# Kernel optimization log

Measured on AMD Instinct MI355X. Metric: run time of the kernel, lower is better.

## Reference

```python
import jax, jax.numpy as jnp
import numpy as np

# GLIF3 / AlphaPSC constants from the module __init__
V_TH = -45.0      # v_threshold
V_RESET = -60.0   # v_reset (also used as leak reversal E_L)
C_M = 2.0         # membrane capacitance
TAU = 20.0        # membrane time constant
TAU_REF = 2.0     # refractory period (ms)
K = np.array([0.1, 0.2], dtype=np.float32)          # after-spike-current decay rates
ASC_AMPS = np.array([1.0, -2.0], dtype=np.float32)  # after-spike-current jump amplitudes
TAU_SYN = 5.0     # alpha synapse time constant
DT = 1.0

T, B, NI, NH, NO = 1000, 32, 512, 1024, 256


def setup_inputs() -> dict:
    key = jax.random.key(0)
    k1, k2, k3, k4 = jax.random.split(key, 4)
    x = jax.random.normal(k1, (T, B, NI), dtype=jnp.float32)
    # fc_in scaled up so injected current actually drives spiking from v_reset to v_threshold
    W_in = jax.random.normal(k2, (NH, NI), dtype=jnp.float32) * (50.0 / np.sqrt(NI))
    W_rec = jax.random.normal(k3, (NH, NH), dtype=jnp.float32) * (1.0 / np.sqrt(NH))
    W_out = jax.random.normal(k4, (NO, NH), dtype=jnp.float32) * (1.0 / np.sqrt(NH))
    return {"x": x, "W_in": W_in, "W_rec": W_rec, "W_out": W_out}


def _spike_fn(v):
    # Heaviside forward, sigmoid surrogate gradient (straight-through)
    soft = jax.nn.sigmoid(4.0 * (v - V_TH))
    hard = (v >= V_TH).astype(v.dtype)
    return soft + jax.lax.stop_gradient(hard - soft)


def reference(x, W_in, W_rec, W_out):
    # fc_in: [T,B,NI] @ [NH,NI]^T -> external current per step [T,B,NH]
    I_ext = jnp.einsum('tbi,hi->tbh', x, W_in)

    decay_syn = jnp.float32(np.exp(-DT / TAU_SYN))
    asc_decay = jnp.exp(-jnp.asarray(K) * DT)          # (2,)
    asc_amps = jnp.asarray(ASC_AMPS)                   # (2,)

    v0 = jnp.full((B, NH), V_RESET, dtype=jnp.float32)
    asc0 = jnp.zeros((2, B, NH), dtype=jnp.float32)
    ref0 = jnp.zeros((B, NH), dtype=jnp.float32)
    h0 = jnp.zeros((B, NH), dtype=jnp.float32)
    psc0 = jnp.zeros((B, NH), dtype=jnp.float32)

    def step(carry, I_t):
        v, asc, ref, h, psc = carry
        I = I_t + psc                                   # external + recurrent synaptic current
        asc = asc * asc_decay[:, None, None]            # after-spike currents decay
        # GLIF membrane update: C dv/dt = -C/tau (v - E_L) + I + sum(asc)
        v = v + DT * ((V_RESET - v) / TAU + (I + asc.sum(0)) / C_M)
        in_ref = ref > 0.0
        v = jnp.where(in_ref, V_RESET, v)               # clamp during refractory
        spike = _spike_fn(v) * (1.0 - in_ref.astype(v.dtype))
        v = v * (1.0 - spike) + V_RESET * spike         # hard reset on spike
        asc = asc + spike[None] * asc_amps[:, None, None]
        ref = jnp.where(spike > 0.5, TAU_REF, jnp.maximum(ref - DT, 0.0))
        # DenseConn recurrent projection of spikes, then AlphaPSC two-state filter
        rec = spike @ W_rec.T
        h = decay_syn * h + rec
        psc = decay_syn * psc + DT * h
        return (v, asc, ref, h, psc), spike

    _, spikes = jax.lax.scan(step, (v0, asc0, ref0, h0, psc0), I_ext)  # spikes: [T,B,NH]
    rate = spikes.mean(axis=0)                          # [B,NH]
    return rate @ W_out.T                               # [B,NO]
```

## Files before the change

kernel.cpp:

```cpp
#include <hip/hip_runtime.h>
#include <stdint.h>

#define T_STEPS 1000
#define B_SZ    32
#define NI      512
#define NH      1024
#define NO      256

#define NSLICE  8
#define NBLK    (B_SZ * NSLICE)

#define NHP     (NH + 16)
#define DUMMY   NH
#define BOFF    544

typedef unsigned long long u64;

#define OFF_IEXT 0ull
#define SZ_IEXT  ((unsigned long long)T_STEPS * B_SZ * NH * 4ull)
#define OFF_WTS  (OFF_IEXT + SZ_IEXT)
#define SZ_WTS   ((unsigned long long)NSLICE * NHP * 128 * 4ull)
#define OFF_RATE (OFF_WTS + SZ_WTS)
#define SZ_RATE  ((unsigned long long)B_SZ * NH * 4ull)
#define OFF_SYNC (OFF_RATE + SZ_RATE)
#define SZ_SYNC  ((unsigned long long)2 * B_SZ * NSLICE * 4 * 8ull)

__device__ __forceinline__ u64 ld64_agent(const u64* p) {
  return __hip_atomic_load(p, __ATOMIC_RELAXED, __HIP_MEMORY_SCOPE_AGENT);
}
__device__ __forceinline__ void st64_agent(u64* p, u64 v) {
  __hip_atomic_store(p, v, __ATOMIC_RELAXED, __HIP_MEMORY_SCOPE_AGENT);
}

__global__ __launch_bounds__(256) void prep_wts(const float* __restrict__ Wrec,
                                                float* __restrict__ WTS) {
  __shared__ float tile[64][65];
  const int tid = threadIdx.x;
  const int j0 = blockIdx.x * 64;
  const int i0 = blockIdx.y * 64;
  const int sl = j0 >> 7;
  const int jjb = j0 & 127;
#pragma unroll
  for (int k = 0; k < 16; ++k) {
    const int idx = k * 256 + tid;
    const int jl = idx >> 6, il = idx & 63;
    tile[jl][il] = Wrec[(size_t)(j0 + jl) * NH + i0 + il];
  }
  __syncthreads();
#pragma unroll
  for (int k = 0; k < 16; ++k) {
    const int idx = k * 256 + tid;
    const int il = idx >> 6, jl = idx & 63;
    WTS[((size_t)(sl * NHP + i0 + il)) * 128 + jjb + jl] = tile[jl][il];
  }
}

#define GBM 128
#define GBN 128
#define GBK 16
__global__ __launch_bounds__(256) void gemm_in(const float* __restrict__ X,
                                               const float* __restrict__ Win,
                                               float* __restrict__ I) {
  __shared__ float As[GBK][GBM + 4];
  __shared__ float Bs[GBK][GBN + 4];
  const int tid = threadIdx.x;
  const int m0 = blockIdx.x * GBM;
  const int n0 = blockIdx.y * GBN;
  const int tm = tid >> 4, tn = tid & 15;
  const int lr = tid >> 1, lk = (tid & 1) * 8;
  float acc[8][8] = {};
  for (int k0 = 0; k0 < NI; k0 += GBK) {
    float4 a0 = *(const float4*)&X[(size_t)(m0 + lr) * NI + k0 + lk];
    float4 a1 = *(const float4*)&X[(size_t)(m0 + lr) * NI + k0 + lk + 4];
    float4 b0 = *(const float4*)&Win[(size_t)(n0 + lr) * NI + k0 + lk];
    float4 b1 = *(const float4*)&Win[(size_t)(n0 + lr) * NI + k0 + lk + 4];
    As[lk + 0][lr] = a0.x; As[lk + 1][lr] = a0.y; As[lk + 2][lr] = a0.z; As[lk + 3][lr] = a0.w;
    As[lk + 4][lr] = a1.x; As[lk + 5][lr] = a1.y; As[lk + 6][lr] = a1.z; As[lk + 7][lr] = a1.w;
    Bs[lk + 0][lr] = b0.x; Bs[lk + 1][lr] = b0.y; Bs[lk + 2][lr] = b0.z; Bs[lk + 3][lr] = b0.w;
    Bs[lk + 4][lr] = b1.x; Bs[lk + 5][lr] = b1.y; Bs[lk + 6][lr] = b1.z; Bs[lk + 7][lr] = b1.w;
    __syncthreads();
#pragma unroll
    for (int k = 0; k < GBK; ++k) {
      float av[8], bv[8];
      *(float4*)&av[0] = *(const float4*)&As[k][tm * 8];
      *(float4*)&av[4] = *(const float4*)&As[k][tm * 8 + 4];
      *(float4*)&bv[0] = *(const float4*)&Bs[k][tn * 8];
      *(float4*)&bv[4] = *(const float4*)&Bs[k][tn * 8 + 4];
#pragma unroll
      for (int i2 = 0; i2 < 8; ++i2)
#pragma unroll
        for (int j2 = 0; j2 < 8; ++j2) acc[i2][j2] += av[i2] * bv[j2];
    }
    __syncthreads();
  }
#pragma unroll
  for (int i2 = 0; i2 < 8; ++i2) {
    float4 c0 = {acc[i2][0], acc[i2][1], acc[i2][2], acc[i2][3]};
    float4 c1 = {acc[i2][4], acc[i2][5], acc[i2][6], acc[i2][7]};
    *(float4*)&I[(size_t)(m0 + tm * 8 + i2) * NH + n0 + tn * 8] = c0;
    *(float4*)&I[(size_t)(m0 + tm * 8 + i2) * NH + n0 + tn * 8 + 4] = c1;
  }
}

__global__ __launch_bounds__(256) void scan_rsnn(const float* __restrict__ Iext,
                                                 const float* __restrict__ WTS,
                                                 float* __restrict__ rate,
                                                 u64* sync) {
  __shared__ unsigned short slist[1088];
  __shared__ int scnt[2];
  __shared__ float psumB[128];

  const int bid = blockIdx.x;
  const int b   = bid >> 3;
  const int sl  = bid & 7;
  const int tid = threadIdx.x;
  const int wv  = tid >> 6;
  const int ln  = tid & 63;
  const int jloc = tid & 127;

  const float* wts = WTS + (size_t)sl * NHP * 128;

  const float D1 = 0.90483741803595957f;
  const float D2 = 0.81873075307798186f;

  float v = -60.0f, A1 = 0.0f, A2 = 0.0f, rf = 0.0f, h = 0.0f, psc = 0.0f;
  float ip = 0.0f;
  int sc = 0;

  if (tid < 128) ip = Iext[(size_t)b * NH + sl * 128 + tid];

  for (int t = 0; t < T_STEPS; ++t) {
    const int par = t & 1;
    u64* gbase = sync + ((size_t)(par * B_SZ + b)) * (NSLICE * 4);

    if (wv < 2) {
      const float I = ip + psc;
      A1 *= D1; A2 *= D2;
      v = v + ((-60.0f - v) / 20.0f + (I + A1 + A2) / 2.0f);
      const bool inref = rf > 0.0f;
      if (inref) v = -60.0f;
      const bool spike = (!inref) && (v >= -45.0f);
      if (spike) { v = -60.0f; A1 += 1.0f; A2 += -2.0f; rf = 2.0f; sc++; }
      else       { rf = fmaxf(rf - 1.0f, 0.0f); }

      const u64 bal = __ballot(spike);
      if (ln < 2) {
        const int w = wv * 2 + ln;
        const unsigned payload = ln ? (unsigned)(bal >> 32) : (unsigned)bal;
        st64_agent(&gbase[sl * 4 + w], (u64)payload | ((u64)(unsigned)(t + 1) << 32));
      }
      __builtin_amdgcn_sched_barrier(0);
      const int tn2 = (t + 1 < T_STEPS) ? t + 1 : t;
      ip = Iext[((size_t)tn2 * B_SZ + b) * NH + sl * 128 + tid];
    } else if (wv == 2) {
      u64 val = 0;
      const u64* gp = &gbase[ln & 31];
      const unsigned want = (unsigned)(t + 1);
      for (;;) {
        if (ln < 32) val = ld64_agent(gp);
        const bool ok = (ln >= 32) || ((unsigned)(val >> 32) == want);
        if (__all(ok)) break;
      }
      unsigned myw = (ln < 32) ? (unsigned)val : 0u;
      int inc = __popc(myw);
#pragma unroll
      for (int d = 1; d < 32; d <<= 1) {
        int y = __shfl_up(inc, d);
        if (ln >= d) inc += y;
      }
      const int cntA = __shfl(inc, 15);
      const int cnt  = __shfl(inc, 31);
      if (ln < 32) {
        int off = inc - __popc(myw);
        if (ln >= 16) off += BOFF - cntA;
        const int base = ln * 32;
        unsigned m = myw;
        while (m) {
          const int bit = __builtin_ctz(m);
          m &= m - 1;
          slist[off++] = (unsigned short)(base + bit);
        }
      }
      const int cB   = cnt - cntA;
      const int cA16 = ((cntA + 15) & ~15) + 16;
      const int cB16 = ((cB   + 15) & ~15) + 16;
      if (ln < cA16 - cntA) slist[cntA + ln]      = (unsigned short)DUMMY;
      if (ln < cB16 - cB)   slist[BOFF + cB + ln] = (unsigned short)DUMMY;
      if (ln == 0) { scnt[0] = cA16; scnt[1] = cB16; }
    }
    __syncthreads();

    float s = 0.0f;
    {
      const int kb   = (tid < 128) ? 0 : BOFF;
      const int kEnd = (tid < 128) ? scnt[0] : scnt[1];
      float wv16[16];
#pragma unroll
      for (int m2 = 0; m2 < 16; ++m2)
        wv16[m2] = wts[(size_t)slist[kb + m2] * 128 + jloc];
      for (int k = 16; k < kEnd; k += 16) {
        float nv16[16];
#pragma unroll
        for (int m2 = 0; m2 < 16; ++m2)
          nv16[m2] = wts[(size_t)slist[kb + k + m2] * 128 + jloc];
#pragma unroll
        for (int m2 = 0; m2 < 16; ++m2) s += wv16[m2];
#pragma unroll
        for (int m2 = 0; m2 < 16; ++m2) wv16[m2] = nv16[m2];
      }
#pragma unroll
      for (int m2 = 0; m2 < 16; ++m2) s += wv16[m2];
    }
    if (tid >= 128) psumB[jloc] = s;
    __syncthreads();

    if (tid < 128) {
      const float rec = s + psumB[tid];
      h = D2 * h + rec;
      psc = D2 * psc + h;
    }
  }

  if (tid < 128) rate[(size_t)b * NH + sl * 128 + tid] = (float)sc / 1000.0f;
}

__global__ __launch_bounds__(256) void out_gemv(const float* __restrict__ rate,
                                                const float* __restrict__ Wout,
                                                float* __restrict__ out) {
  __shared__ float rs[NH];
  const int b = blockIdx.x, tid = threadIdx.x;
  for (int i = tid; i < NH; i += 256) rs[i] = rate[(size_t)b * NH + i];
  __syncthreads();
  const float* wr = Wout + (size_t)tid * NH;
  float s = 0.0f;
  for (int hh = 0; hh < NH; hh += 4) {
    float4 w4 = *(const float4*)&wr[hh];
    s += rs[hh] * w4.x + rs[hh + 1] * w4.y + rs[hh + 2] * w4.z + rs[hh + 3] * w4.w;
  }
  out[(size_t)b * NO + tid] = s;
}

extern "C" void kernel_launch(void* const* d_in, const int* in_sizes, int n_in,
                              void* d_out, int out_size, void* d_ws, size_t ws_size,
                              hipStream_t stream) {
  const float* x    = (const float*)d_in[0];
  const float* Win  = (const float*)d_in[1];
  const float* Wrec = (const float*)d_in[2];
  const float* Wout = (const float*)d_in[3];
  float* out = (float*)d_out;

  char* ws = (char*)d_ws;
  float* Iext = (float*)(ws + OFF_IEXT);
  float* WTS  = (float*)(ws + OFF_WTS);
  float* rate = (float*)(ws + OFF_RATE);
  u64*   sync = (u64*)(ws + OFF_SYNC);

  hipMemsetAsync(ws + OFF_WTS, 0, SZ_WTS, stream);

  prep_wts<<<dim3(16, 16), dim3(256), 0, stream>>>(Wrec, WTS);
  gemm_in<<<dim3((T_STEPS * B_SZ) / GBM, NH / GBN), dim3(256), 0, stream>>>(x, Win, Iext);
  scan_rsnn<<<dim3(NBLK), dim3(256), 0, stream>>>(Iext, WTS, rate, sync);
  out_gemv<<<dim3(B_SZ), dim3(256), 0, stream>>>(rate, Wout, out);
}
```

Measured before the change: 3.600 ms.

## Split scan into 16 slices with warp-specialized roles and LDS flag handoffs

The recurrent scan now uses 16 neuron slices of 64 per batch (512 units), packed two units per 512-thread block. Inside each unit the block-wide __syncthreads is replaced by warp-specialized roles: one wavefront runs neuron updates, one polls global spike bitmasks and builds the spike list, and two accumulate weight sums. They hand off through workgroup-scope release/acquire flags in LDS. The aim is to shorten the per-step critical path, letting the gather and list-building steps overlap and spreading the weight sums over more CUs. In exchange, each batch row now waits on twice as many slices and polls with spin loops using s_sleep.

```diff
diff --git a/kernel.cpp b/kernel.cpp
--- a/kernel.cpp
+++ b/kernel.cpp
@@ -7,8 +7,9 @@
 #define NH      1024
 #define NO      256
 
-#define NSLICE  8
-#define NBLK    (B_SZ * NSLICE)
+#define NSLICE  16
+#define NUNIT   (B_SZ * NSLICE)
+#define NBLK    256
 
 #define NHP     (NH + 16)
 #define DUMMY   NH
@@ -19,11 +20,11 @@
 #define OFF_IEXT 0ull
 #define SZ_IEXT  ((unsigned long long)T_STEPS * B_SZ * NH * 4ull)
 #define OFF_WTS  (OFF_IEXT + SZ_IEXT)
-#define SZ_WTS   ((unsigned long long)NSLICE * NHP * 128 * 4ull)
+#define SZ_WTS   ((unsigned long long)NSLICE * NHP * 64 * 4ull)
 #define OFF_RATE (OFF_WTS + SZ_WTS)
 #define SZ_RATE  ((unsigned long long)B_SZ * NH * 4ull)
 #define OFF_SYNC (OFF_RATE + SZ_RATE)
-#define SZ_SYNC  ((unsigned long long)2 * B_SZ * NSLICE * 4 * 8ull)
+#define SZ_SYNC  ((unsigned long long)2 * B_SZ * 32 * 8ull)
 
 __device__ __forceinline__ u64 ld64_agent(const u64* p) {
   return __hip_atomic_load(p, __ATOMIC_RELAXED, __HIP_MEMORY_SCOPE_AGENT);
@@ -31,15 +32,29 @@
 __device__ __forceinline__ void st64_agent(u64* p, u64 v) {
   __hip_atomic_store(p, v, __ATOMIC_RELAXED, __HIP_MEMORY_SCOPE_AGENT);
 }
+__device__ __forceinline__ void sigl(int* f, int v) {
+  __hip_atomic_store(f, v, __ATOMIC_RELEASE, __HIP_MEMORY_SCOPE_WORKGROUP);
+}
+__device__ __forceinline__ void waitl(int* f, int v) {
+  while (__hip_atomic_load(f, __ATOMIC_ACQUIRE, __HIP_MEMORY_SCOPE_WORKGROUP) < v) {
+    __builtin_amdgcn_s_sleep(1);
+  }
+}
+
+#define FL  0
+#define FGA 1
+#define FGB 2
+#define FPA 3
+#define FPB 4
+#define FC  5
 
 __global__ __launch_bounds__(256) void prep_wts(const float* __restrict__ Wrec,
                                                 float* __restrict__ WTS) {
   __shared__ float tile[64][65];
   const int tid = threadIdx.x;
-  const int j0 = blockIdx.x * 64;
+  const int s  = blockIdx.x;
+  const int j0 = s * 64;
   const int i0 = blockIdx.y * 64;
-  const int sl = j0 >> 7;
-  const int jjb = j0 & 127;
 #pragma unroll
   for (int k = 0; k < 16; ++k) {
     const int idx = k * 256 + tid;
@@ -51,7 +66,7 @@
   for (int k = 0; k < 16; ++k) {
     const int idx = k * 256 + tid;
     const int il = idx >> 6, jl = idx & 63;
-    WTS[((size_t)(sl * NHP + i0 + il)) * 128 + jjb + jl] = tile[jl][il];
+    WTS[((size_t)(s * NHP + i0 + il)) * 64 + jl] = tile[jl][il];
   }
 }
 
@@ -102,38 +117,42 @@
   }
 }
 
-__global__ __launch_bounds__(256) void scan_rsnn(const float* __restrict__ Iext,
+__global__ __launch_bounds__(512) void scan_rsnn(const float* __restrict__ Iext,
                                                  const float* __restrict__ WTS,
                                                  float* __restrict__ rate,
                                                  u64* sync) {
-  __shared__ unsigned short slist[1088];
-  __shared__ int scnt[2];
-  __shared__ float psumB[128];
-
-  const int bid = blockIdx.x;
-  const int b   = bid >> 3;
-  const int sl  = bid & 7;
-  const int tid = threadIdx.x;
-  const int wv  = tid >> 6;
-  const int ln  = tid & 63;
-  const int jloc = tid & 127;
-
-  const float* wts = WTS + (size_t)sl * NHP * 128;
+  __shared__ unsigned short slist[2][1088];
+  __shared__ int   scnt[2][2];
+  __shared__ float psumA[2][64];
+  __shared__ float psumB[2][64];
+  __shared__ int   flg[2][8];
+
+  const int tid  = threadIdx.x;
+  const int sub  = tid >> 8;
+  const int stid = tid & 255;
+  const int wr   = stid >> 6;
+  const int ln   = stid & 63;
+
+  const int u  = blockIdx.x + (sub << 8);
+  const int b  = u >> 4;
+  const int sl = u & 15;
+  const int j0 = sl * 64;
+
+  const float* wts = WTS + (size_t)sl * NHP * 64;
+  int* fl = flg[sub];
+
+  if (tid < 16) ((int*)flg)[tid] = 0;
+  __syncthreads();
 
   const float D1 = 0.90483741803595957f;
   const float D2 = 0.81873075307798186f;
 
-  float v = -60.0f, A1 = 0.0f, A2 = 0.0f, rf = 0.0f, h = 0.0f, psc = 0.0f;
-  float ip = 0.0f;
-  int sc = 0;
-
-  if (tid < 128) ip = Iext[(size_t)b * NH + sl * 128 + tid];
-
-  for (int t = 0; t < T_STEPS; ++t) {
-    const int par = t & 1;
-    u64* gbase = sync + ((size_t)(par * B_SZ + b)) * (NSLICE * 4);
-
-    if (wv < 2) {
+  if (wr == 0) {
+    float v = -60.0f, A1 = 0.0f, A2 = 0.0f, rf = 0.0f, h = 0.0f, psc = 0.0f;
+    int sc = 0;
+    float ip = Iext[(size_t)b * NH + j0 + ln];
+    for (int t = 0; t < T_STEPS; ++t) {
+      u64* gbase = sync + ((size_t)((t & 1) * B_SZ + b)) * 32;
       const float I = ip + psc;
       A1 *= D1; A2 *= D2;
       v = v + ((-60.0f - v) / 20.0f + (I + A1 + A2) / 2.0f);
@@ -142,17 +161,27 @@
       const bool spike = (!inref) && (v >= -45.0f);
       if (spike) { v = -60.0f; A1 += 1.0f; A2 += -2.0f; rf = 2.0f; sc++; }
       else       { rf = fmaxf(rf - 1.0f, 0.0f); }
-
       const u64 bal = __ballot(spike);
       if (ln < 2) {
-        const int w = wv * 2 + ln;
         const unsigned payload = ln ? (unsigned)(bal >> 32) : (unsigned)bal;
-        st64_agent(&gbase[sl * 4 + w], (u64)payload | ((u64)(unsigned)(t + 1) << 32));
+        st64_agent(&gbase[sl * 2 + ln], (u64)payload | ((u64)(unsigned)(t + 1) << 32));
       }
       __builtin_amdgcn_sched_barrier(0);
       const int tn2 = (t + 1 < T_STEPS) ? t + 1 : t;
-      ip = Iext[((size_t)tn2 * B_SZ + b) * NH + sl * 128 + tid];
-    } else if (wv == 2) {
+      ip = Iext[((size_t)tn2 * B_SZ + b) * NH + j0 + ln];
+      waitl(&fl[FPA], t + 1);
+      waitl(&fl[FPB], t + 1);
+      const float rec = psumA[sub][ln] + psumB[sub][ln];
+      h = D2 * h + rec;
+      psc = D2 * psc + h;
+      if (ln == 0) sigl(&fl[FC], t + 1);
+    }
+    rate[(size_t)b * NH + j0 + ln] = (float)sc / 1000.0f;
+
+  } else if (wr == 1) {
+    for (int t = 0; t < T_STEPS; ++t) {
+      u64* gbase = sync + ((size_t)((t & 1) * B_SZ + b)) * 32;
+      if (t) { waitl(&fl[FGA], t); waitl(&fl[FGB], t); }
       u64 val = 0;
       const u64* gp = &gbase[ln & 31];
       const unsigned want = (unsigned)(t + 1);
@@ -178,31 +207,33 @@
         while (m) {
           const int bit = __builtin_ctz(m);
           m &= m - 1;
-          slist[off++] = (unsigned short)(base + bit);
+          slist[sub][off++] = (unsigned short)(base + bit);
         }
       }
       const int cB   = cnt - cntA;
       const int cA16 = ((cntA + 15) & ~15) + 16;
       const int cB16 = ((cB   + 15) & ~15) + 16;
-      if (ln < cA16 - cntA) slist[cntA + ln]      = (unsigned short)DUMMY;
-      if (ln < cB16 - cB)   slist[BOFF + cB + ln] = (unsigned short)DUMMY;
-      if (ln == 0) { scnt[0] = cA16; scnt[1] = cB16; }
-    }
-    __syncthreads();
-
-    float s = 0.0f;
-    {
-      const int kb   = (tid < 128) ? 0 : BOFF;
-      const int kEnd = (tid < 128) ? scnt[0] : scnt[1];
+      if (ln < cA16 - cntA) slist[sub][cntA + ln]      = (unsigned short)DUMMY;
+      if (ln < cB16 - cB)   slist[sub][BOFF + cB + ln] = (unsigned short)DUMMY;
+      if (ln == 0) { scnt[sub][0] = cA16; scnt[sub][1] = cB16; }
+      if (ln == 0) sigl(&fl[FL], t + 1);
+    }
+
+  } else {
+    const int kb = (wr == 2) ? 0 : BOFF;
+    for (int t = 0; t < T_STEPS; ++t) {
+      waitl(&fl[FL], t + 1);
+      const int kEnd = scnt[sub][wr - 2];
+      float s = 0.0f;
       float wv16[16];
 #pragma unroll
       for (int m2 = 0; m2 < 16; ++m2)
-        wv16[m2] = wts[(size_t)slist[kb + m2] * 128 + jloc];
+        wv16[m2] = wts[(size_t)slist[sub][kb + m2] * 64 + ln];
       for (int k = 16; k < kEnd; k += 16) {
         float nv16[16];
 #pragma unroll
         for (int m2 = 0; m2 < 16; ++m2)
-          nv16[m2] = wts[(size_t)slist[kb + k + m2] * 128 + jloc];
+          nv16[m2] = wts[(size_t)slist[sub][kb + k + m2] * 64 + ln];
 #pragma unroll
         for (int m2 = 0; m2 < 16; ++m2) s += wv16[m2];
 #pragma unroll
@@ -210,18 +241,12 @@
       }
 #pragma unroll
       for (int m2 = 0; m2 < 16; ++m2) s += wv16[m2];
-    }
-    if (tid >= 128) psumB[jloc] = s;
-    __syncthreads();
-
-    if (tid < 128) {
-      const float rec = s + psumB[tid];
-      h = D2 * h + rec;
-      psc = D2 * psc + h;
-    }
-  }
-
-  if (tid < 128) rate[(size_t)b * NH + sl * 128 + tid] = (float)sc / 1000.0f;
+      if (ln == 0) sigl(wr == 2 ? &fl[FGA] : &fl[FGB], t + 1);
+      if (t) waitl(&fl[FC], t);
+      if (wr == 2) psumA[sub][ln] = s; else psumB[sub][ln] = s;
+      if (ln == 0) sigl(wr == 2 ? &fl[FPA] : &fl[FPB], t + 1);
+    }
+  }
 }
 
 __global__ __launch_bounds__(256) void out_gemv(const float* __restrict__ rate,
@@ -259,6 +284,6 @@
 
   prep_wts<<<dim3(16, 16), dim3(256), 0, stream>>>(Wrec, WTS);
   gemm_in<<<dim3((T_STEPS * B_SZ) / GBM, NH / GBN), dim3(256), 0, stream>>>(x, Win, Iext);
-  scan_rsnn<<<dim3(NBLK), dim3(256), 0, stream>>>(Iext, WTS, rate, sync);
+  scan_rsnn<<<dim3(NBLK), dim3(512), 0, stream>>>(Iext, WTS, rate, sync);
   out_gemv<<<dim3(B_SZ), dim3(256), 0, stream>>>(rate, Wout, out);
 }
```

Measured after the change: 4.876 ms. +35.5%, slower.

## Split recurrent scan into 16 slices per batch with cooperative launch and fallback

Applied to the files above, without the earlier changes.

Doubles the number of neuron slices per batch row to 16, so 512 blocks each own 64 neurons. One wave runs the neuron update, one builds the spike list, and two waves gather recurrent weights. The weight layout is changed to 64-column slices, and the launch is cooperative so all blocks are guaranteed co-resident for the spin-wait sync. A fallback 8-slice kernel handles the case where the cooperative launch fails. The aim is to spread the serial per-step work across more CUs; the cost is more blocks polling sync flags, two per CU, plus a staggered start via s_sleep.

```diff
diff --git a/kernel.cpp b/kernel.cpp
--- a/kernel.cpp
+++ b/kernel.cpp
@@ -7,8 +7,9 @@
 #define NH      1024
 #define NO      256
 
-#define NSLICE  8
+#define NSLICE  16
 #define NBLK    (B_SZ * NSLICE)
+#define NBLK_FB 256
 
 #define NHP     (NH + 16)
 #define DUMMY   NH
@@ -19,11 +20,11 @@
 #define OFF_IEXT 0ull
 #define SZ_IEXT  ((unsigned long long)T_STEPS * B_SZ * NH * 4ull)
 #define OFF_WTS  (OFF_IEXT + SZ_IEXT)
-#define SZ_WTS   ((unsigned long long)NSLICE * NHP * 128 * 4ull)
+#define SZ_WTS   ((unsigned long long)NSLICE * NHP * 64 * 4ull)
 #define OFF_RATE (OFF_WTS + SZ_WTS)
 #define SZ_RATE  ((unsigned long long)B_SZ * NH * 4ull)
 #define OFF_SYNC (OFF_RATE + SZ_RATE)
-#define SZ_SYNC  ((unsigned long long)2 * B_SZ * NSLICE * 4 * 8ull)
+#define SZ_SYNC  ((unsigned long long)2 * B_SZ * 32 * 8ull)
 
 __device__ __forceinline__ u64 ld64_agent(const u64* p) {
   return __hip_atomic_load(p, __ATOMIC_RELAXED, __HIP_MEMORY_SCOPE_AGENT);
@@ -36,10 +37,9 @@
                                                 float* __restrict__ WTS) {
   __shared__ float tile[64][65];
   const int tid = threadIdx.x;
-  const int j0 = blockIdx.x * 64;
+  const int s  = blockIdx.x;
+  const int j0 = s * 64;
   const int i0 = blockIdx.y * 64;
-  const int sl = j0 >> 7;
-  const int jjb = j0 & 127;
 #pragma unroll
   for (int k = 0; k < 16; ++k) {
     const int idx = k * 256 + tid;
@@ -51,7 +51,7 @@
   for (int k = 0; k < 16; ++k) {
     const int idx = k * 256 + tid;
     const int il = idx >> 6, jl = idx & 63;
-    WTS[((size_t)(sl * NHP + i0 + il)) * 128 + jjb + jl] = tile[jl][il];
+    WTS[((size_t)(s * NHP + i0 + il)) * 64 + jl] = tile[jl][il];
   }
 }
 
@@ -102,23 +102,23 @@
   }
 }
 
-__global__ __launch_bounds__(256) void scan_rsnn(const float* __restrict__ Iext,
-                                                 const float* __restrict__ WTS,
-                                                 float* __restrict__ rate,
-                                                 u64* sync) {
+__global__ __launch_bounds__(256, 2) void scan_coop(const float* __restrict__ Iext,
+                                                    const float* __restrict__ WTS,
+                                                    float* __restrict__ rate,
+                                                    u64* sync) {
   __shared__ unsigned short slist[1088];
   __shared__ int scnt[2];
-  __shared__ float psumB[128];
+  __shared__ float psumA[64];
+  __shared__ float psumB[64];
 
   const int bid = blockIdx.x;
-  const int b   = bid >> 3;
-  const int sl  = bid & 7;
+  const int b   = bid >> 4;
+  const int sl  = bid & 15;
   const int tid = threadIdx.x;
   const int wv  = tid >> 6;
   const int ln  = tid & 63;
-  const int jloc = tid & 127;
-
-  const float* wts = WTS + (size_t)sl * NHP * 128;
+
+  const float* wts = WTS + (size_t)sl * NHP * 64;
 
   const float D1 = 0.90483741803595957f;
   const float D2 = 0.81873075307798186f;
@@ -127,13 +127,15 @@
   float ip = 0.0f;
   int sc = 0;
 
-  if (tid < 128) ip = Iext[(size_t)b * NH + sl * 128 + tid];
+  if (wv == 0) ip = Iext[(size_t)b * NH + sl * 64 + ln];
+
+  if (b & 16) __builtin_amdgcn_s_sleep(45);
 
   for (int t = 0; t < T_STEPS; ++t) {
     const int par = t & 1;
-    u64* gbase = sync + ((size_t)(par * B_SZ + b)) * (NSLICE * 4);
-
-    if (wv < 2) {
+    u64* gbase = sync + ((size_t)(par * B_SZ + b)) * 32;
+
+    if (wv == 0) {
       const float I = ip + psc;
       A1 *= D1; A2 *= D2;
       v = v + ((-60.0f - v) / 20.0f + (I + A1 + A2) / 2.0f);
@@ -145,14 +147,13 @@
 
       const u64 bal = __ballot(spike);
       if (ln < 2) {
-        const int w = wv * 2 + ln;
         const unsigned payload = ln ? (unsigned)(bal >> 32) : (unsigned)bal;
-        st64_agent(&gbase[sl * 4 + w], (u64)payload | ((u64)(unsigned)(t + 1) << 32));
+        st64_agent(&gbase[sl * 2 + ln], (u64)payload | ((u64)(unsigned)(t + 1) << 32));
       }
       __builtin_amdgcn_sched_barrier(0);
       const int tn2 = (t + 1 < T_STEPS) ? t + 1 : t;
-      ip = Iext[((size_t)tn2 * B_SZ + b) * NH + sl * 128 + tid];
-    } else if (wv == 2) {
+      ip = Iext[((size_t)tn2 * B_SZ + b) * NH + sl * 64 + ln];
+    } else if (wv == 1) {
       u64 val = 0;
       const u64* gp = &gbase[ln & 31];
       const unsigned want = (unsigned)(t + 1);
@@ -190,6 +191,128 @@
     }
     __syncthreads();
 
+    if (wv >= 2) {
+      const int kb   = (wv == 2) ? 0 : BOFF;
+      const int kEnd = (wv == 2) ? scnt[0] : scnt[1];
+      float s = 0.0f;
+      float wv16[16];
+#pragma unroll
+      for (int m2 = 0; m2 < 16; ++m2)
+        wv16[m2] = wts[(size_t)slist[kb + m2] * 64 + ln];
+      for (int k = 16; k < kEnd; k += 16) {
+        float nv16[16];
+#pragma unroll
+        for (int m2 = 0; m2 < 16; ++m2)
+          nv16[m2] = wts[(size_t)slist[kb + k + m2] * 64 + ln];
+#pragma unroll
+        for (int m2 = 0; m2 < 16; ++m2) s += wv16[m2];
+#pragma unroll
+        for (int m2 = 0; m2 < 16; ++m2) wv16[m2] = nv16[m2];
+      }
+#pragma unroll
+      for (int m2 = 0; m2 < 16; ++m2) s += wv16[m2];
+      if (wv == 2) psumA[ln] = s; else psumB[ln] = s;
+    }
+    __syncthreads();
+
+    if (wv == 0) {
+      const float rec = psumA[ln] + psumB[ln];
+      h = D2 * h + rec;
+      psc = D2 * psc + h;
+    }
+  }
+
+  if (wv == 0) rate[(size_t)b * NH + sl * 64 + ln] = (float)sc / 1000.0f;
+}
+
+__global__ __launch_bounds__(256) void scan_fb(const float* __restrict__ Iext,
+                                               const float* __restrict__ WTS,
+                                               float* __restrict__ rate,
+                                               u64* sync) {
+  __shared__ unsigned short slist[1088];
+  __shared__ int scnt[2];
+  __shared__ float psumB[128];
+
+  const int bid = blockIdx.x;
+  const int b   = bid >> 3;
+  const int sl  = bid & 7;
+  const int tid = threadIdx.x;
+  const int wv  = tid >> 6;
+  const int ln  = tid & 63;
+  const int jloc = tid & 127;
+
+  const float* wtsf = WTS + (size_t)(sl * 2 + (jloc >> 6)) * NHP * 64 + (jloc & 63);
+
+  const float D1 = 0.90483741803595957f;
+  const float D2 = 0.81873075307798186f;
+
+  float v = -60.0f, A1 = 0.0f, A2 = 0.0f, rf = 0.0f, h = 0.0f, psc = 0.0f;
+  float ip = 0.0f;
+  int sc = 0;
+
+  if (tid < 128) ip = Iext[(size_t)b * NH + sl * 128 + tid];
+
+  for (int t = 0; t < T_STEPS; ++t) {
+    const int par = t & 1;
+    u64* gbase = sync + ((size_t)(par * B_SZ + b)) * 32;
+
+    if (wv < 2) {
+      const float I = ip + psc;
+      A1 *= D1; A2 *= D2;
+      v = v + ((-60.0f - v) / 20.0f + (I + A1 + A2) / 2.0f);
+      const bool inref = rf > 0.0f;
+      if (inref) v = -60.0f;
+      const bool spike = (!inref) && (v >= -45.0f);
+      if (spike) { v = -60.0f; A1 += 1.0f; A2 += -2.0f; rf = 2.0f; sc++; }
+      else       { rf = fmaxf(rf - 1.0f, 0.0f); }
+
+      const u64 bal = __ballot(spike);
+      if (ln < 2) {
+        const int w = wv * 2 + ln;
+        const unsigned payload = ln ? (unsigned)(bal >> 32) : (unsigned)bal;
+        st64_agent(&gbase[sl * 4 + w], (u64)payload | ((u64)(unsigned)(t + 1) << 32));
+      }
+      __builtin_amdgcn_sched_barrier(0);
+      const int tn2 = (t + 1 < T_STEPS) ? t + 1 : t;
+      ip = Iext[((size_t)tn2 * B_SZ + b) * NH + sl * 128 + tid];
+    } else if (wv == 2) {
+      u64 val = 0;
+      const u64* gp = &gbase[ln & 31];
+      const unsigned want = (unsigned)(t + 1);
+      for (;;) {
+        if (ln < 32) val = ld64_agent(gp);
+        const bool ok = (ln >= 32) || ((unsigned)(val >> 32) == want);
+        if (__all(ok)) break;
+      }
+      unsigned myw = (ln < 32) ? (unsigned)val : 0u;
+      int inc = __popc(myw);
+#pragma unroll
+      for (int d = 1; d < 32; d <<= 1) {
+        int y = __shfl_up(inc, d);
+        if (ln >= d) inc += y;
+      }
+      const int cntA = __shfl(inc, 15);
+      const int cnt  = __shfl(inc, 31);
+      if (ln < 32) {
+        int off = inc - __popc(myw);
+        if (ln >= 16) off += BOFF - cntA;
+        const int base = ln * 32;
+        unsigned m = myw;
+        while (m) {
+          const int bit = __builtin_ctz(m);
+          m &= m - 1;
+          slist[off++] = (unsigned short)(base + bit);
+        }
+      }
+      const int cB   = cnt - cntA;
+      const int cA16 = ((cntA + 15) & ~15) + 16;
+      const int cB16 = ((cB   + 15) & ~15) + 16;
+      if (ln < cA16 - cntA) slist[cntA + ln]      = (unsigned short)DUMMY;
+      if (ln < cB16 - cB)   slist[BOFF + cB + ln] = (unsigned short)DUMMY;
+      if (ln == 0) { scnt[0] = cA16; scnt[1] = cB16; }
+    }
+    __syncthreads();
+
     float s = 0.0f;
     {
       const int kb   = (tid < 128) ? 0 : BOFF;
@@ -197,12 +320,12 @@
       float wv16[16];
 #pragma unroll
       for (int m2 = 0; m2 < 16; ++m2)
-        wv16[m2] = wts[(size_t)slist[kb + m2] * 128 + jloc];
+        wv16[m2] = wtsf[(size_t)slist[kb + m2] * 64];
       for (int k = 16; k < kEnd; k += 16) {
         float nv16[16];
 #pragma unroll
         for (int m2 = 0; m2 < 16; ++m2)
-          nv16[m2] = wts[(size_t)slist[kb + k + m2] * 128 + jloc];
+          nv16[m2] = wtsf[(size_t)slist[kb + k + m2] * 64];
 #pragma unroll
         for (int m2 = 0; m2 < 16; ++m2) s += wv16[m2];
 #pragma unroll
@@ -257,8 +380,19 @@
 
   hipMemsetAsync(ws + OFF_WTS, 0, SZ_WTS, stream);
 
-  prep_wts<<<dim3(16, 16), dim3(256), 0, stream>>>(Wrec, WTS);
+  prep_wts<<<dim3(NSLICE, 16), dim3(256), 0, stream>>>(Wrec, WTS);
   gemm_in<<<dim3((T_STEPS * B_SZ) / GBM, NH / GBN), dim3(256), 0, stream>>>(x, Win, Iext);
-  scan_rsnn<<<dim3(NBLK), dim3(256), 0, stream>>>(Iext, WTS, rate, sync);
+
+  {
+    void* args[] = {(void*)&Iext, (void*)&WTS, (void*)&rate, (void*)&sync};
+    hipError_t e = hipLaunchCooperativeKernel((const void*)scan_coop,
+                                              dim3(NBLK), dim3(256),
+                                              args, 0, stream);
+    if (e != hipSuccess) {
+      (void)hipGetLastError();
+      scan_fb<<<dim3(NBLK_FB), dim3(256), 0, stream>>>(Iext, WTS, rate, sync);
+    }
+  }
+
   out_gemv<<<dim3(B_SZ), dim3(256), 0, stream>>>(rate, Wout, out);
 }
```

New measurement: 4.533 ms. 25.9% more time.

## Process two batch rows per block and overlap polling with gather

Applied to the files above, without the earlier changes.

Each block now handles two batch elements (b and b+16), halving the grid to 128 blocks. The second batch's spike-poll and compaction run on one wave while the other waves gather weights for the first batch, so inter-block sync latency overlaps with gather work. The B-half gather is done by a single wave using float2 loads. This trades per-block parallelism and adds an extra barrier per step in exchange for fewer co-resident blocks spinning on sync and better latency hiding.

```diff
diff --git a/kernel.cpp b/kernel.cpp
--- a/kernel.cpp
+++ b/kernel.cpp
@@ -8,11 +8,15 @@
 #define NO      256
 
 #define NSLICE  8
-#define NBLK    (B_SZ * NSLICE)
+#define NGRP    16
+#define NBLK    (NGRP * NSLICE)
 
 #define NHP     (NH + 16)
 #define DUMMY   NH
 #define BOFF    544
+
+#define D1C 0.90483741803595957f
+#define D2C 0.81873075307798186f
 
 typedef unsigned long long u64;
 
@@ -102,126 +106,185 @@
   }
 }
 
+
+__device__ __forceinline__ void state_pub(float& v, float& A1, float& A2, float& rf,
+                                          const float psc, const float ip, int& sc,
+                                          u64* gb, const int sl, const int wv,
+                                          const int ln, const int t) {
+  const float I = ip + psc;
+  A1 *= D1C; A2 *= D2C;
+  v = v + ((-60.0f - v) / 20.0f + (I + A1 + A2) / 2.0f);
+  const bool inref = rf > 0.0f;
+  if (inref) v = -60.0f;
+  const bool spike = (!inref) && (v >= -45.0f);
+  if (spike) { v = -60.0f; A1 += 1.0f; A2 += -2.0f; rf = 2.0f; sc++; }
+  else       { rf = fmaxf(rf - 1.0f, 0.0f); }
+  const u64 bal = __ballot(spike);
+  if (ln < 2) {
+    const int w = wv * 2 + ln;
+    const unsigned payload = ln ? (unsigned)(bal >> 32) : (unsigned)bal;
+    st64_agent(&gb[sl * 4 + w], (u64)payload | ((u64)(unsigned)(t + 1) << 32));
+  }
+}
+
+__device__ __forceinline__ void poll_compact(u64* gbase, const unsigned want,
+                                             const int ln,
+                                             unsigned short* sl_, int* sc_) {
+  u64 val = 0;
+  const u64* gp = &gbase[ln & 31];
+  for (;;) {
+    if (ln < 32) val = ld64_agent(gp);
+    const bool ok = (ln >= 32) || ((unsigned)(val >> 32) == want);
+    if (__all(ok)) break;
+  }
+  unsigned myw = (ln < 32) ? (unsigned)val : 0u;
+  int inc = __popc(myw);
+#pragma unroll
+  for (int d = 1; d < 32; d <<= 1) {
+    int y = __shfl_up(inc, d);
+    if (ln >= d) inc += y;
+  }
+  const int cntA = __shfl(inc, 15);
+  const int cnt  = __shfl(inc, 31);
+  if (ln < 32) {
+    int off = inc - __popc(myw);
+    if (ln >= 16) off += BOFF - cntA;
+    const int base = ln * 32;
+    unsigned m = myw;
+    while (m) {
+      const int bit = __builtin_ctz(m);
+      m &= m - 1;
+      sl_[off++] = (unsigned short)(base + bit);
+    }
+  }
+  const int cB   = cnt - cntA;
+  const int cA16 = ((cntA + 15) & ~15) + 16;
+  const int cB16 = ((cB   + 15) & ~15) + 16;
+  if (ln < cA16 - cntA) sl_[cntA + ln]      = (unsigned short)DUMMY;
+  if (ln < cB16 - cB)   sl_[BOFF + cB + ln] = (unsigned short)DUMMY;
+  if (ln == 0) { sc_[0] = cA16; sc_[1] = cB16; }
+}
+
+__device__ __forceinline__ float gather_A(const float* wts, const unsigned short* sl_,
+                                          const int kEnd, const int jloc) {
+  float s = 0.0f;
+  float wv16[16];
+#pragma unroll
+  for (int m2 = 0; m2 < 16; ++m2)
+    wv16[m2] = wts[(size_t)sl_[m2] * 128 + jloc];
+  for (int k = 16; k < kEnd; k += 16) {
+    float nv16[16];
+#pragma unroll
+    for (int m2 = 0; m2 < 16; ++m2)
+      nv16[m2] = wts[(size_t)sl_[k + m2] * 128 + jloc];
+#pragma unroll
+    for (int m2 = 0; m2 < 16; ++m2) s += wv16[m2];
+#pragma unroll
+    for (int m2 = 0; m2 < 16; ++m2) wv16[m2] = nv16[m2];
+  }
+#pragma unroll
+  for (int m2 = 0; m2 < 16; ++m2) s += wv16[m2];
+  return s;
+}
+
+__device__ __forceinline__ void gather_B2(const float* wts, const unsigned short* sl_,
+                                          const int kEnd, const int ln, float* ps) {
+  float sx = 0.0f, sy = 0.0f;
+  const unsigned short* lb = sl_ + BOFF;
+  float2 wv16[16];
+#pragma unroll
+  for (int m2 = 0; m2 < 16; ++m2)
+    wv16[m2] = *(const float2*)&wts[(size_t)lb[m2] * 128 + 2 * ln];
+  for (int k = 16; k < kEnd; k += 16) {
+    float2 nv16[16];
+#pragma unroll
+    for (int m2 = 0; m2 < 16; ++m2)
+      nv16[m2] = *(const float2*)&wts[(size_t)lb[k + m2] * 128 + 2 * ln];
+#pragma unroll
+    for (int m2 = 0; m2 < 16; ++m2) { sx += wv16[m2].x; sy += wv16[m2].y; }
+#pragma unroll
+    for (int m2 = 0; m2 < 16; ++m2) wv16[m2] = nv16[m2];
+  }
+#pragma unroll
+  for (int m2 = 0; m2 < 16; ++m2) { sx += wv16[m2].x; sy += wv16[m2].y; }
+  ps[2 * ln]     = sx;
+  ps[2 * ln + 1] = sy;
+}
+
 __global__ __launch_bounds__(256) void scan_rsnn(const float* __restrict__ Iext,
                                                  const float* __restrict__ WTS,
                                                  float* __restrict__ rate,
                                                  u64* sync) {
-  __shared__ unsigned short slist[1088];
-  __shared__ int scnt[2];
-  __shared__ float psumB[128];
+  __shared__ unsigned short slist[2][1088];
+  __shared__ int   scnt[2][2];
+  __shared__ float psum[2][128];
 
   const int bid = blockIdx.x;
-  const int b   = bid >> 3;
+  const int g   = bid >> 3;
   const int sl  = bid & 7;
+  const int bX  = g;
+  const int bY  = g + 16;
   const int tid = threadIdx.x;
   const int wv  = tid >> 6;
   const int ln  = tid & 63;
-  const int jloc = tid & 127;
 
   const float* wts = WTS + (size_t)sl * NHP * 128;
 
-  const float D1 = 0.90483741803595957f;
-  const float D2 = 0.81873075307798186f;
-
-  float v = -60.0f, A1 = 0.0f, A2 = 0.0f, rf = 0.0f, h = 0.0f, psc = 0.0f;
-  float ip = 0.0f;
-  int sc = 0;
-
-  if (tid < 128) ip = Iext[(size_t)b * NH + sl * 128 + tid];
+  float vX = -60.0f, A1X = 0.0f, A2X = 0.0f, rfX = 0.0f, hX = 0.0f, pscX = 0.0f, ipX = 0.0f;
+  float vY = -60.0f, A1Y = 0.0f, A2Y = 0.0f, rfY = 0.0f, hY = 0.0f, pscY = 0.0f, ipY = 0.0f;
+  int scX = 0, scY = 0;
+
+  if (tid < 128) {
+    ipX = Iext[(size_t)bX * NH + sl * 128 + tid];
+    ipY = Iext[(size_t)bY * NH + sl * 128 + tid];
+  }
 
   for (int t = 0; t < T_STEPS; ++t) {
     const int par = t & 1;
-    u64* gbase = sync + ((size_t)(par * B_SZ + b)) * (NSLICE * 4);
-
-    if (wv < 2) {
-      const float I = ip + psc;
-      A1 *= D1; A2 *= D2;
-      v = v + ((-60.0f - v) / 20.0f + (I + A1 + A2) / 2.0f);
-      const bool inref = rf > 0.0f;
-      if (inref) v = -60.0f;
-      const bool spike = (!inref) && (v >= -45.0f);
-      if (spike) { v = -60.0f; A1 += 1.0f; A2 += -2.0f; rf = 2.0f; sc++; }
-      else       { rf = fmaxf(rf - 1.0f, 0.0f); }
-
-      const u64 bal = __ballot(spike);
-      if (ln < 2) {
-        const int w = wv * 2 + ln;
-        const unsigned payload = ln ? (unsigned)(bal >> 32) : (unsigned)bal;
-        st64_agent(&gbase[sl * 4 + w], (u64)payload | ((u64)(unsigned)(t + 1) << 32));
-      }
+    const unsigned want = (unsigned)(t + 1);
+    u64* gX = sync + ((size_t)(par * B_SZ + bX)) * (NSLICE * 4);
+    u64* gY = sync + ((size_t)(par * B_SZ + bY)) * (NSLICE * 4);
+
+    if (tid < 128) {
+      state_pub(vX, A1X, A2X, rfX, pscX, ipX, scX, gX, sl, wv, ln, t);
+      state_pub(vY, A1Y, A2Y, rfY, pscY, ipY, scY, gY, sl, wv, ln, t);
       __builtin_amdgcn_sched_barrier(0);
       const int tn2 = (t + 1 < T_STEPS) ? t + 1 : t;
-      ip = Iext[((size_t)tn2 * B_SZ + b) * NH + sl * 128 + tid];
+      ipX = Iext[((size_t)tn2 * B_SZ + bX) * NH + sl * 128 + tid];
+      ipY = Iext[((size_t)tn2 * B_SZ + bY) * NH + sl * 128 + tid];
     } else if (wv == 2) {
-      u64 val = 0;
-      const u64* gp = &gbase[ln & 31];
-      const unsigned want = (unsigned)(t + 1);
-      for (;;) {
-        if (ln < 32) val = ld64_agent(gp);
-        const bool ok = (ln >= 32) || ((unsigned)(val >> 32) == want);
-        if (__all(ok)) break;
-      }
-      unsigned myw = (ln < 32) ? (unsigned)val : 0u;
-      int inc = __popc(myw);
-#pragma unroll
-      for (int d = 1; d < 32; d <<= 1) {
-        int y = __shfl_up(inc, d);
-        if (ln >= d) inc += y;
-      }
-      const int cntA = __shfl(inc, 15);
-      const int cnt  = __shfl(inc, 31);
-      if (ln < 32) {
-        int off = inc - __popc(myw);
-        if (ln >= 16) off += BOFF - cntA;
-        const int base = ln * 32;
-        unsigned m = myw;
-        while (m) {
-          const int bit = __builtin_ctz(m);
-          m &= m - 1;
-          slist[off++] = (unsigned short)(base + bit);
-        }
-      }
-      const int cB   = cnt - cntA;
-      const int cA16 = ((cntA + 15) & ~15) + 16;
-      const int cB16 = ((cB   + 15) & ~15) + 16;
-      if (ln < cA16 - cntA) slist[cntA + ln]      = (unsigned short)DUMMY;
-      if (ln < cB16 - cB)   slist[BOFF + cB + ln] = (unsigned short)DUMMY;
-      if (ln == 0) { scnt[0] = cA16; scnt[1] = cB16; }
-    }
-    __syncthreads();
-
-    float s = 0.0f;
-    {
-      const int kb   = (tid < 128) ? 0 : BOFF;
-      const int kEnd = (tid < 128) ? scnt[0] : scnt[1];
-      float wv16[16];
-#pragma unroll
-      for (int m2 = 0; m2 < 16; ++m2)
-        wv16[m2] = wts[(size_t)slist[kb + m2] * 128 + jloc];
-      for (int k = 16; k < kEnd; k += 16) {
-        float nv16[16];
-#pragma unroll
-        for (int m2 = 0; m2 < 16; ++m2)
-          nv16[m2] = wts[(size_t)slist[kb + k + m2] * 128 + jloc];
-#pragma unroll
-        for (int m2 = 0; m2 < 16; ++m2) s += wv16[m2];
-#pragma unroll
-        for (int m2 = 0; m2 < 16; ++m2) wv16[m2] = nv16[m2];
-      }
-#pragma unroll
-      for (int m2 = 0; m2 < 16; ++m2) s += wv16[m2];
-    }
-    if (tid >= 128) psumB[jloc] = s;
-    __syncthreads();
-
+      poll_compact(gX, want, ln, slist[0], scnt[0]);
+    }
+    __syncthreads();
+
+    float sAX = 0.0f;
+    if (tid < 128)       sAX = gather_A(wts, slist[0], scnt[0][0], tid);
+    else if (wv == 3)    gather_B2(wts, slist[0], scnt[0][1], ln, psum[0]);
+    else    poll_compact(gY, want, ln, slist[1], scnt[1]);
+    __syncthreads();
+
+    float sAY = 0.0f;
     if (tid < 128) {
-      const float rec = s + psumB[tid];
-      h = D2 * h + rec;
-      psc = D2 * psc + h;
-    }
-  }
-
-  if (tid < 128) rate[(size_t)b * NH + sl * 128 + tid] = (float)sc / 1000.0f;
+      const float recX = sAX + psum[0][tid];
+      hX = D2C * hX + recX;
+      pscX = D2C * pscX + hX;
+      sAY = gather_A(wts, slist[1], scnt[1][0], tid);
+    } else if (wv == 3) {
+      gather_B2(wts, slist[1], scnt[1][1], ln, psum[1]);
+    }
+    __syncthreads();
+
+    if (tid < 128) {
+      const float recY = sAY + psum[1][tid];
+      hY = D2C * hY + recY;
+      pscY = D2C * pscY + hY;
+    }
+  }
+
+  if (tid < 128) {
+    rate[(size_t)bX * NH + sl * 128 + tid] = (float)scX / 1000.0f;
+    rate[(size_t)bY * NH + sl * 128 + tid] = (float)scY / 1000.0f;
+  }
 }
 
 __global__ __launch_bounds__(256) void out_gemv(const float* __restrict__ rate,
```

Result: slower. 5.430 ms (+50.8%).
